# Optimization experiments

Hardware: AMD Instinct MI355X
Metric: run time of the kernel (lower is better)

The kernel has to match this reference:

```python
import jax, jax.numpy as jnp
import numpy as np

B, S, D, H = 4, 2048, 1024, 16
DK = D // H

def setup_inputs() -> dict:
    key = jax.random.key(0)
    ks = jax.random.split(key, 12)
    s = 1.0 / np.sqrt(D)
    return {
        "query": jax.random.normal(ks[0], (B, S, D), jnp.float32),
        "key": jax.random.normal(ks[1], (B, S, D), jnp.float32),
        "value": jax.random.normal(ks[2], (B, S, D), jnp.float32),
        "mask": jax.random.randint(ks[3], (B, S, S), 0, 2, jnp.int32),
        "Wq": jax.random.normal(ks[4], (D, D), jnp.float32) * s,
        "bq": jnp.zeros((D,), jnp.float32),
        "Wk": jax.random.normal(ks[5], (D, D), jnp.float32) * s,
        "bk": jnp.zeros((D,), jnp.float32),
        "Wv": jax.random.normal(ks[6], (D, D), jnp.float32) * s,
        "bv": jnp.zeros((D,), jnp.float32),
        "Wo": jax.random.normal(ks[7], (D, D), jnp.float32) * s,
        "bo": jnp.zeros((D,), jnp.float32),
    }

def _split_heads(x):
    b, s, _ = x.shape
    return x.reshape(b, s, H, DK).transpose(0, 2, 1, 3)  # [b,h,s,dk]

def reference(query, key, value, mask, Wq, bq, Wk, bk, Wv, bv, Wo, bo):
    # torch nn.Linear: y = x @ W.T + b
    Q = _split_heads(query @ Wq.T + bq)
    K = _split_heads(key @ Wk.T + bk)
    V = _split_heads(value @ Wv.T + bv)
    scores = jnp.einsum('bhqd,bhkd->bhqk', Q, K) / np.sqrt(DK)
    scores = jnp.where(mask[:, None, :, :] == 0, jnp.float32(-1e9), scores)
    probs = jax.nn.softmax(scores, axis=-1)
    attn = jnp.einsum('bhqk,bhkd->bhqd', probs, V)
    out = attn.transpose(0, 2, 1, 3).reshape(query.shape[0], -1, H * DK)
    return out @ Wo.T + bo
```

## Files before the change

kernel.cpp:

```cpp
#include <hip/hip_runtime.h>

typedef __attribute__((ext_vector_type(8))) short short8;
typedef __attribute__((ext_vector_type(8))) unsigned short ushort8_t;
typedef __attribute__((ext_vector_type(4))) float floatx4;
typedef __attribute__((ext_vector_type(2))) _Float16 half2_t;
typedef __attribute__((ext_vector_type(4))) _Float16 half4;
typedef __attribute__((ext_vector_type(8))) _Float16 half8;
typedef __attribute__((ext_vector_type(2))) unsigned int uint2v;

#define B_ 4
#define S_ 2048
#define D_ 1024
#define H_ 16
#define DK_ 64
#define BS_ (B_ * S_)
#define XN4_ (BS_ * D_ / 4)
#define WN4_ (D_ * D_ / 4)

union V8u { half8 v8; half4 v4[2]; };
union H16 { _Float16 h; unsigned short u; };

typedef const __attribute__((address_space(1))) void* gvp;
typedef __attribute__((address_space(3))) void* lvp;

static __device__ __forceinline__ unsigned short f2bf(float f) {
  union { float f; unsigned int u; } x; x.f = f;
  unsigned int r = x.u + 0x7fffu + ((x.u >> 16) & 1u);
  return (unsigned short)(r >> 16);
}

static __device__ __forceinline__ half2_t pk_f16(float a, float b) {
  return __builtin_bit_cast(half2_t, __builtin_amdgcn_cvt_pkrtz(a, b));
}

static __device__ __forceinline__ float fexp2(float x) {
  float r;
  asm("v_exp_f32 %0, %1" : "=v"(r) : "v"(x));
  return r;
}

static __device__ __forceinline__ half8 mk8(uint2v a, uint2v b) {
  union { unsigned u[4]; half8 h; } t;
  t.u[0] = a.x; t.u[1] = a.y; t.u[2] = b.x; t.u[3] = b.y;
  return t.h;
}

__global__ void cast_all(const float* __restrict__ q, const float* __restrict__ k,
                         const float* __restrict__ v,
                         const float* __restrict__ wq, const float* __restrict__ wk,
                         const float* __restrict__ wv, const float* __restrict__ wo,
                         unsigned short* __restrict__ oq, unsigned short* __restrict__ ok,
                         unsigned short* __restrict__ ov,
                         unsigned short* __restrict__ owq, unsigned short* __restrict__ owk,
                         unsigned short* __restrict__ owv, unsigned short* __restrict__ owo) {
  int i = blockIdx.x * blockDim.x + threadIdx.x;
  const float* src; unsigned short* dst; int j;
  if (i < 3 * XN4_) {
    int w = i >> 21; j = i & (XN4_ - 1);
    src = (w == 0) ? q : (w == 1) ? k : v;
    dst = (w == 0) ? oq : (w == 1) ? ok : ov;
  } else {
    int t = i - 3 * XN4_;
    int w = t >> 18; j = t & (WN4_ - 1);
    src = (w == 0) ? wq : (w == 1) ? wk : (w == 2) ? wv : wo;
    dst = (w == 0) ? owq : (w == 1) ? owk : (w == 2) ? owv : owo;
  }
  float4 v4 = ((const float4*)src)[j];
  ushort4 o;
  o.x = f2bf(v4.x); o.y = f2bf(v4.y); o.z = f2bf(v4.z); o.w = f2bf(v4.w);
  ((ushort4*)dst)[j] = o;
}

__global__ void pack_mask(const int* __restrict__ mask, unsigned long long* __restrict__ bits) {
  int i = blockIdx.x * blockDim.x + threadIdx.x;
  unsigned long long m = __ballot(mask[i] != 0);
  if ((threadIdx.x & 63) == 0) bits[i >> 6] = m;
}

__device__ __forceinline__ void gemm_core(
    const unsigned short* __restrict__ X, const unsigned short* __restrict__ W,
    const float* __restrict__ bias, void* __restrict__ Y,
    float scale, int mode, int bm, int bn,
    unsigned short* As, unsigned short* Bs)
{
  constexpr int K = D_, N = D_;
  int tid = threadIdx.x;
  int wave = tid >> 6, lane = tid & 63, quad = lane >> 4, li = lane & 15;
  int wm = wave >> 1, wn = wave & 1;
  int srow = lane >> 3;
  int scol = ((lane & 7) ^ srow) * 8;
  const unsigned short* gA = X + (size_t)(bm * 128 + wave * 32 + srow) * K + scol;
  const unsigned short* gB = W + (size_t)(bn * 128 + wave * 32 + srow) * K + scol;

  auto stage = [&](int buf, int k0) {
#pragma unroll
    for (int j = 0; j < 4; ++j) {
      __builtin_amdgcn_global_load_lds((gvp)(gA + (size_t)(j * 8) * K + k0),
          (lvp)(As + buf * 8192 + wave * 2048 + j * 512), 16, 0, 0);
      __builtin_amdgcn_global_load_lds((gvp)(gB + (size_t)(j * 8) * K + k0),
          (lvp)(Bs + buf * 8192 + wave * 2048 + j * 512), 16, 0, 0);
    }
  };

  floatx4 acc[4][4] = {};
  stage(0, 0);
  constexpr int NK = K / 64;
  for (int i = 0; i < NK; ++i) {
    int buf = i & 1;
    __syncthreads();
    if (i + 1 < NK) stage(buf ^ 1, (i + 1) * 64);
    short8 af[2][4], bf[2][4];
#pragma unroll
    for (int s2 = 0; s2 < 2; ++s2)
#pragma unroll
      for (int t = 0; t < 4; ++t) {
        int slot = ((s2 * 4 + quad) ^ (li & 7)) * 8;
        af[s2][t] = *(const short8*)(&As[buf * 8192 + (wm * 64 + t * 16 + li) * 64 + slot]);
        bf[s2][t] = *(const short8*)(&Bs[buf * 8192 + (wn * 64 + t * 16 + li) * 64 + slot]);
      }
#pragma unroll
    for (int s2 = 0; s2 < 2; ++s2)
#pragma unroll
      for (int mt = 0; mt < 4; ++mt)
#pragma unroll
        for (int nt = 0; nt < 4; ++nt)
          acc[mt][nt] = __builtin_amdgcn_mfma_f32_16x16x32_bf16(af[s2][mt], bf[s2][nt], acc[mt][nt], 0, 0, 0);
  }

  if (mode == 3) {
    int mbase = bm * 128 + wm * 64;
    int b0 = mbase >> 11;
    int sblk = mbase & 2047;
#pragma unroll
    for (int nt = 0; nt < 4; ++nt) {
      int n = bn * 128 + wn * 64 + nt * 16 + li;
      float bv = bias[n];
      int h = n >> 6, dk = n & 63;
#pragma unroll
      for (int mt = 0; mt < 4; ++mt) {
        int pos = (mt >> 1) * 32 + quad * 8 + (mt & 1) * 4;
        H16 h0, h1, h2, h3;
        h0.h = (_Float16)(acc[mt][nt][0] + bv);
        h1.h = (_Float16)(acc[mt][nt][1] + bv);
        h2.h = (_Float16)(acc[mt][nt][2] + bv);
        h3.h = (_Float16)(acc[mt][nt][3] + bv);
        uint2v pk;
        pk.x = (unsigned)h0.u | ((unsigned)h1.u << 16);
        pk.y = (unsigned)h2.u | ((unsigned)h3.u << 16);
        size_t idx = (((size_t)(b0 * H_ + h)) * DK_ + dk) * S_ + sblk + pos;
        *(uint2v*)((unsigned short*)Y + idx) = pk;
      }
    }
    return;
  }

#pragma unroll
  for (int nt = 0; nt < 4; ++nt) {
    int n = bn * 128 + wn * 64 + nt * 16 + li;
    float bv = bias[n];
#pragma unroll
    for (int mt = 0; mt < 4; ++mt) {
#pragma unroll
      for (int r = 0; r < 4; ++r) {
        int m = bm * 128 + wm * 64 + mt * 16 + quad * 4 + r;
        float v = (acc[mt][nt][r] + bv) * scale;
        if (mode == 1) {
          ((float*)Y)[(size_t)m * N + n] = v;
        } else {
          int b = m >> 11, s = m & 2047, h = n >> 6, dk = n & 63;
          size_t idx = (((size_t)(b * H_ + h)) * S_ + s) * DK_ + dk;
          ((unsigned short*)Y)[idx] = f2bf(v);
        }
      }
    }
  }
}

__global__ __launch_bounds__(256) void gemm_qkv(
    const unsigned short* __restrict__ Xq, const unsigned short* __restrict__ Xk,
    const unsigned short* __restrict__ Xv,
    const unsigned short* __restrict__ Wq, const unsigned short* __restrict__ Wk,
    const unsigned short* __restrict__ Wv,
    const float* __restrict__ bq, const float* __restrict__ bk, const float* __restrict__ bv,
    unsigned short* __restrict__ Qh, unsigned short* __restrict__ Kh,
    unsigned short* __restrict__ Vt, float sc)
{
  __shared__ __align__(16) unsigned short As[2 * 8192];
  __shared__ __align__(16) unsigned short Bs[2 * 8192];
  int z = blockIdx.z;
  const unsigned short* X = (z == 0) ? Xq : (z == 1) ? Xk : Xv;
  const unsigned short* W = (z == 0) ? Wq : (z == 1) ? Wk : Wv;
  const float* bias = (z == 0) ? bq : (z == 1) ? bk : bv;
  void* Y = (z == 0) ? (void*)Qh : (z == 1) ? (void*)Kh : (void*)Vt;
  float scale = (z == 0) ? sc : 1.0f;
  int mode = (z == 2) ? 3 : 0;
  gemm_core(X, W, bias, Y, scale, mode, blockIdx.y, blockIdx.x, As, Bs);
}

__global__ __launch_bounds__(256) void gemm_out(
    const unsigned short* __restrict__ X, const unsigned short* __restrict__ W,
    const float* __restrict__ bias, float* __restrict__ Y)
{
  __shared__ __align__(16) unsigned short As[2 * 8192];
  __shared__ __align__(16) unsigned short Bs[2 * 8192];
  gemm_core(X, W, bias, Y, 1.0f, 1, blockIdx.y, blockIdx.x, As, Bs);
}

__global__ __launch_bounds__(256) void attn_kernel(
    const unsigned short* __restrict__ Qh,
    const unsigned short* __restrict__ Kh,
    const _Float16* __restrict__ Vt,
    const unsigned long long* __restrict__ mbits,
    unsigned short* __restrict__ attnb)
{
  __shared__ __align__(16) unsigned short Ks[2 * 4096];
  __shared__ __align__(16) unsigned short Vs[2 * 4096];
  __shared__ __align__(8) uint2v mlut[16];

  int tid = threadIdx.x;
  int wave = tid >> 6, lane = tid & 63, quad = lane >> 4, li = lane & 15;

  if (tid < 16) {
    unsigned nb = (unsigned)tid;
    uint2v m;
    m.x = (nb & 1u ? 0x0000FFFFu : 0u) | (nb & 2u ? 0xFFFF0000u : 0u);
    m.y = (nb & 4u ? 0x0000FFFFu : 0u) | (nb & 8u ? 0xFFFF0000u : 0u);
    mlut[nb] = m;
  }

  int blk = blockIdx.x;
  int xcd = blk & 7, slot7 = blk >> 3;
  int bh = xcd * 8 + (slot7 >> 4);
  int qb = slot7 & 15;
  int b = bh >> 4, h = bh & 15;
  int qbase = qb * 128 + wave * 32;
  const size_t hq = (size_t)bh * S_ * DK_;

  short8 aQ[2][2];
#pragma unroll
  for (int qs = 0; qs < 2; ++qs)
#pragma unroll
    for (int s2 = 0; s2 < 2; ++s2)
      aQ[qs][s2] = *(const short8*)(Qh + hq + (size_t)(qbase + qs * 16 + li) * DK_ + s2 * 32 + quad * 8);

  floatx4 o[2][4] = {};
  floatx4 lacc[2] = {};
  const half8 ones8 = {(_Float16)1.f, (_Float16)1.f, (_Float16)1.f, (_Float16)1.f,
                       (_Float16)1.f, (_Float16)1.f, (_Float16)1.f, (_Float16)1.f};

  const unsigned long long* mrow = mbits + ((size_t)b * S_ + qbase + li) * (S_ / 64);

  int srow = lane >> 3;
  int scol = ((lane & 7) ^ srow) * 8;
  const unsigned short* gK = Kh + hq + (size_t)(wave * 16 + srow) * DK_ + scol;
  const _Float16* gV = Vt + ((size_t)bh * 64 + wave * 16 + srow) * S_ + scol;

  auto stage = [&](int buf, int k0) {
#pragma unroll
    for (int j = 0; j < 2; ++j) {
      __builtin_amdgcn_global_load_lds((gvp)(gK + (size_t)(k0 + j * 8) * DK_),
          (lvp)(Ks + buf * 4096 + wave * 1024 + j * 512), 16, 0, 0);
      __builtin_amdgcn_global_load_lds((gvp)(gV + (size_t)(j * 8) * S_ + k0),
          (lvp)(Vs + buf * 4096 + wave * 1024 + j * 512), 16, 0, 0);
    }
  };

  stage(0, 0);
  unsigned long long mw0c = mrow[0];
  unsigned long long mw1c = mrow[16 * (S_ / 64)];

  constexpr int NK = S_ / 64;
#pragma unroll 2
  for (int i = 0; i < NK; ++i) {
    int buf = i & 1;
    __syncthreads();
    if (i + 1 < NK) stage(buf ^ 1, (i + 1) * 64);
    unsigned long long mw0n = 0, mw1n = 0;
    if (i + 1 < NK) { mw0n = mrow[i + 1]; mw1n = mrow[16 * (S_ / 64) + i + 1]; }

    short8 bK[4][2];
#pragma unroll
    for (int t = 0; t < 4; ++t)
#pragma unroll
      for (int s2 = 0; s2 < 2; ++s2)
        bK[t][s2] = *(const short8*)(&Ks[buf * 4096 + (t * 16 + li) * 64 + (((s2 * 4 + quad) ^ (li & 7)) * 8)]);

    V8u vv[4][2];
#pragma unroll
    for (int dt = 0; dt < 4; ++dt)
#pragma unroll
      for (int tp = 0; tp < 2; ++tp)
        vv[dt][tp].v8 = *(const half8*)((const _Float16*)&Vs[buf * 4096 + (dt * 16 + li) * 64 + (((tp * 4 + quad) ^ (li & 7)) * 8)]);

    floatx4 sc[4][2] = {};
    __builtin_amdgcn_s_setprio(1);
#pragma unroll
    for (int s2 = 0; s2 < 2; ++s2)
#pragma unroll
      for (int t = 0; t < 4; ++t)
#pragma unroll
        for (int qs = 0; qs < 2; ++qs)
          sc[t][qs] = __builtin_amdgcn_mfma_f32_16x16x32_bf16(bK[t][s2], aQ[qs][s2], sc[t][qs], 0, 0, 0);
    __builtin_amdgcn_s_setprio(0);

    unsigned long long sh0 = mw0c >> (quad * 4);
    unsigned long long sh1 = mw1c >> (quad * 4);

    uint2v aPu[4][2];
#pragma unroll
    for (int t = 0; t < 4; ++t)
#pragma unroll
      for (int qs = 0; qs < 2; ++qs) {
        unsigned nb = (unsigned)(((qs ? sh1 : sh0) >> (t * 16)) & 15u);
        uint2v mm = mlut[nb];
        float p0 = fexp2(sc[t][qs][0]);
        float p1 = fexp2(sc[t][qs][1]);
        float p2 = fexp2(sc[t][qs][2]);
        float p3 = fexp2(sc[t][qs][3]);
        uint2v pp;
        pp.x = __builtin_bit_cast(unsigned, pk_f16(p0, p1)) & mm.x;
        pp.y = __builtin_bit_cast(unsigned, pk_f16(p2, p3)) & mm.y;
        aPu[t][qs] = pp;
      }

    __builtin_amdgcn_s_setprio(1);
#pragma unroll
    for (int a = 0; a < 2; ++a)
#pragma unroll
      for (int qs = 0; qs < 2; ++qs) {
        half8 pa = mk8(aPu[2 * a][qs], aPu[2 * a + 1][qs]);
        lacc[qs] = __builtin_amdgcn_mfma_f32_16x16x32_f16(pa, ones8, lacc[qs], 0, 0, 0);
#pragma unroll
        for (int dt = 0; dt < 4; ++dt)
          o[qs][dt] = __builtin_amdgcn_mfma_f32_16x16x32_f16(pa, vv[dt][a].v8, o[qs][dt], 0, 0, 0);
      }
    __builtin_amdgcn_s_setprio(0);

    mw0c = mw0n; mw1c = mw1n;
  }

#pragma unroll
  for (int qs = 0; qs < 2; ++qs)
#pragma unroll
    for (int r = 0; r < 4; ++r) {
      float ir = 1.0f / lacc[qs][r];
      size_t row = (size_t)b * S_ + qbase + qs * 16 + quad * 4 + r;
#pragma unroll
      for (int dt = 0; dt < 4; ++dt)
        attnb[row * D_ + h * DK_ + dt * 16 + li] = f2bf(o[qs][dt][r] * ir);
    }
}

extern "C" void kernel_launch(void* const* d_in, const int* in_sizes, int n_in,
                              void* d_out, int out_size, void* d_ws, size_t ws_size,
                              hipStream_t stream) {
  const float* query = (const float*)d_in[0];
  const float* key   = (const float*)d_in[1];
  const float* value = (const float*)d_in[2];
  const int*   mask  = (const int*)d_in[3];
  const float* Wq = (const float*)d_in[4];
  const float* bq = (const float*)d_in[5];
  const float* Wk = (const float*)d_in[6];
  const float* bk = (const float*)d_in[7];
  const float* Wv = (const float*)d_in[8];
  const float* bv = (const float*)d_in[9];
  const float* Wo = (const float*)d_in[10];
  const float* bo = (const float*)d_in[11];
  float* out = (float*)d_out;

  char* ws = (char*)d_ws;
  size_t off = 0;
  auto alloc = [&](size_t bytes) -> void* {
    void* p = ws + off;
    off += (bytes + 255) & ~(size_t)255;
    return p;
  };
  unsigned short* Xq    = (unsigned short*)alloc((size_t)BS_ * D_ * 2);
  unsigned short* Xk    = (unsigned short*)alloc((size_t)BS_ * D_ * 2);
  unsigned short* Xv    = (unsigned short*)alloc((size_t)BS_ * D_ * 2);
  unsigned short* Wqb   = (unsigned short*)alloc((size_t)D_ * D_ * 2);
  unsigned short* Wkb   = (unsigned short*)alloc((size_t)D_ * D_ * 2);
  unsigned short* Wvb   = (unsigned short*)alloc((size_t)D_ * D_ * 2);
  unsigned short* Wob   = (unsigned short*)alloc((size_t)D_ * D_ * 2);
  unsigned short* Qh    = (unsigned short*)alloc((size_t)BS_ * D_ * 2);
  unsigned short* Kh    = (unsigned short*)alloc((size_t)BS_ * D_ * 2);
  unsigned short* Vt    = (unsigned short*)alloc((size_t)BS_ * D_ * 2);
  unsigned short* attnb = (unsigned short*)alloc((size_t)BS_ * D_ * 2);
  unsigned long long* mbits = (unsigned long long*)alloc((size_t)B_ * S_ * (S_ / 64) * 8);

  const float SC = 0.18033688011112042f;

  pack_mask<<<(B_ * S_ * S_) / 256, 256, 0, stream>>>(mask, mbits);

  cast_all<<<(3 * XN4_ + 4 * WN4_) / 256, 256, 0, stream>>>(
      query, key, value, Wq, Wk, Wv, Wo,
      Xq, Xk, Xv, Wqb, Wkb, Wvb, Wob);

  gemm_qkv<<<dim3(D_ / 128, BS_ / 128, 3), 256, 0, stream>>>(
      Xq, Xk, Xv, Wqb, Wkb, Wvb, bq, bk, bv, Qh, Kh, Vt, SC);

  attn_kernel<<<dim3(8 * 8 * 16), 256, 0, stream>>>(Qh, Kh, (const _Float16*)Vt, mbits, attnb);

  gemm_out<<<dim3(D_ / 128, BS_ / 128), 256, 0, stream>>>(attnb, Wob, bo, out);
}
```

Before: 415.2 us.

## Fuse fp32-to-bf16 activation cast into QKV GEMM A-tile staging

Drops the separate cast of the query, key and value activations to bf16. The QKV GEMM now reads fp32 rows straight into registers, converts them with packed bf16 conversion and writes the tile to LDS. The A-tile store is issued after the MFMA loop to overlap with compute. This avoids writing and re-reading three large bf16 intermediates, but the GEMM now reads twice as many A bytes through registers rather than direct global-to-LDS loads, which uses more VGPRs and may hurt latency hiding. The rounding also changes from the manual round-to-nearest-even routine to the hardware packed conversion.

Result: slower. 442.1 us (+6.5%).

```diff
diff --git a/kernel.cpp b/kernel.cpp
--- a/kernel.cpp
+++ b/kernel.cpp
@@ -14,7 +14,6 @@
 #define H_ 16
 #define DK_ 64
 #define BS_ (B_ * S_)
-#define XN4_ (BS_ * D_ / 4)
 #define WN4_ (D_ * D_ / 4)
 
 union V8u { half8 v8; half4 v4[2]; };
@@ -29,6 +28,12 @@
   return (unsigned short)(r >> 16);
 }
 
+static __device__ __forceinline__ unsigned cvtpk_bf16(float a, float b) {
+  unsigned r;
+  asm("v_cvt_pk_bf16_f32 %0, %1, %2" : "=v"(r) : "v"(a), "v"(b));
+  return r;
+}
+
 static __device__ __forceinline__ half2_t pk_f16(float a, float b) {
   return __builtin_bit_cast(half2_t, __builtin_amdgcn_cvt_pkrtz(a, b));
 }
@@ -45,26 +50,14 @@
   return t.h;
 }
 
-__global__ void cast_all(const float* __restrict__ q, const float* __restrict__ k,
-                         const float* __restrict__ v,
-                         const float* __restrict__ wq, const float* __restrict__ wk,
-                         const float* __restrict__ wv, const float* __restrict__ wo,
-                         unsigned short* __restrict__ oq, unsigned short* __restrict__ ok,
-                         unsigned short* __restrict__ ov,
-                         unsigned short* __restrict__ owq, unsigned short* __restrict__ owk,
-                         unsigned short* __restrict__ owv, unsigned short* __restrict__ owo) {
+__global__ void cast_w(const float* __restrict__ wq, const float* __restrict__ wk,
+                       const float* __restrict__ wv, const float* __restrict__ wo,
+                       unsigned short* __restrict__ owq, unsigned short* __restrict__ owk,
+                       unsigned short* __restrict__ owv, unsigned short* __restrict__ owo) {
   int i = blockIdx.x * blockDim.x + threadIdx.x;
-  const float* src; unsigned short* dst; int j;
-  if (i < 3 * XN4_) {
-    int w = i >> 21; j = i & (XN4_ - 1);
-    src = (w == 0) ? q : (w == 1) ? k : v;
-    dst = (w == 0) ? oq : (w == 1) ? ok : ov;
-  } else {
-    int t = i - 3 * XN4_;
-    int w = t >> 18; j = t & (WN4_ - 1);
-    src = (w == 0) ? wq : (w == 1) ? wk : (w == 2) ? wv : wo;
-    dst = (w == 0) ? owq : (w == 1) ? owk : (w == 2) ? owv : owo;
-  }
+  int w = i >> 18, j = i & (WN4_ - 1);
+  const float* src = (w == 0) ? wq : (w == 1) ? wk : (w == 2) ? wv : wo;
+  unsigned short* dst = (w == 0) ? owq : (w == 1) ? owk : (w == 2) ? owv : owo;
   float4 v4 = ((const float4*)src)[j];
   ushort4 o;
   o.x = f2bf(v4.x); o.y = f2bf(v4.y); o.z = f2bf(v4.z); o.w = f2bf(v4.w);
@@ -77,8 +70,9 @@
   if ((threadIdx.x & 63) == 0) bits[i >> 6] = m;
 }
 
+template <bool AF32>
 __device__ __forceinline__ void gemm_core(
-    const unsigned short* __restrict__ X, const unsigned short* __restrict__ W,
+    const void* __restrict__ Xp, const unsigned short* __restrict__ W,
     const float* __restrict__ bias, void* __restrict__ Y,
     float scale, int mode, int bm, int bn,
     unsigned short* As, unsigned short* Bs)
@@ -89,26 +83,57 @@
   int wm = wave >> 1, wn = wave & 1;
   int srow = lane >> 3;
   int scol = ((lane & 7) ^ srow) * 8;
-  const unsigned short* gA = X + (size_t)(bm * 128 + wave * 32 + srow) * K + scol;
+  const unsigned short* gA16 = (const unsigned short*)Xp + (size_t)(bm * 128 + wave * 32 + srow) * K + scol;
+  const float*          gA32 = (const float*)Xp          + (size_t)(bm * 128 + wave * 32 + srow) * K + scol;
   const unsigned short* gB = W + (size_t)(bn * 128 + wave * 32 + srow) * K + scol;
 
-  auto stage = [&](int buf, int k0) {
-#pragma unroll
-    for (int j = 0; j < 4; ++j) {
-      __builtin_amdgcn_global_load_lds((gvp)(gA + (size_t)(j * 8) * K + k0),
-          (lvp)(As + buf * 8192 + wave * 2048 + j * 512), 16, 0, 0);
+  auto stageB = [&](int buf, int k0) {
+#pragma unroll
+    for (int j = 0; j < 4; ++j)
       __builtin_amdgcn_global_load_lds((gvp)(gB + (size_t)(j * 8) * K + k0),
           (lvp)(Bs + buf * 8192 + wave * 2048 + j * 512), 16, 0, 0);
+  };
+  auto stageA16 = [&](int buf, int k0) {
+#pragma unroll
+    for (int j = 0; j < 4; ++j)
+      __builtin_amdgcn_global_load_lds((gvp)(gA16 + (size_t)(j * 8) * K + k0),
+          (lvp)(As + buf * 8192 + wave * 2048 + j * 512), 16, 0, 0);
+  };
+
+  float4 fa0[4], fa1[4];
+  auto loadA32 = [&](int k0) {
+#pragma unroll
+    for (int j = 0; j < 4; ++j) {
+      fa0[j] = *(const float4*)(gA32 + (size_t)(j * 8) * K + k0);
+      fa1[j] = *(const float4*)(gA32 + (size_t)(j * 8) * K + k0 + 4);
+    }
+  };
+  auto writeA32 = [&](int buf) {
+#pragma unroll
+    for (int j = 0; j < 4; ++j) {
+      uint4 p;
+      p.x = cvtpk_bf16(fa0[j].x, fa0[j].y);
+      p.y = cvtpk_bf16(fa0[j].z, fa0[j].w);
+      p.z = cvtpk_bf16(fa1[j].x, fa1[j].y);
+      p.w = cvtpk_bf16(fa1[j].z, fa1[j].w);
+      *(uint4*)(&As[buf * 8192 + wave * 2048 + j * 512 + lane * 8]) = p;
     }
   };
 
   floatx4 acc[4][4] = {};
-  stage(0, 0);
+  stageB(0, 0);
+  if (AF32) { loadA32(0); writeA32(0); }
+  else stageA16(0, 0);
+
   constexpr int NK = K / 64;
   for (int i = 0; i < NK; ++i) {
     int buf = i & 1;
     __syncthreads();
-    if (i + 1 < NK) stage(buf ^ 1, (i + 1) * 64);
+    if (i + 1 < NK) {
+      stageB(buf ^ 1, (i + 1) * 64);
+      if (AF32) loadA32((i + 1) * 64);
+      else stageA16(buf ^ 1, (i + 1) * 64);
+    }
     short8 af[2][4], bf[2][4];
 #pragma unroll
     for (int s2 = 0; s2 < 2; ++s2)
@@ -125,6 +150,7 @@
 #pragma unroll
         for (int nt = 0; nt < 4; ++nt)
           acc[mt][nt] = __builtin_amdgcn_mfma_f32_16x16x32_bf16(af[s2][mt], bf[s2][nt], acc[mt][nt], 0, 0, 0);
+    if (AF32 && i + 1 < NK) writeA32(buf ^ 1);
   }
 
   if (mode == 3) {
@@ -177,8 +203,8 @@
 }
 
 __global__ __launch_bounds__(256) void gemm_qkv(
-    const unsigned short* __restrict__ Xq, const unsigned short* __restrict__ Xk,
-    const unsigned short* __restrict__ Xv,
+    const float* __restrict__ Xq, const float* __restrict__ Xk,
+    const float* __restrict__ Xv,
     const unsigned short* __restrict__ Wq, const unsigned short* __restrict__ Wk,
     const unsigned short* __restrict__ Wv,
     const float* __restrict__ bq, const float* __restrict__ bk, const float* __restrict__ bv,
@@ -188,13 +214,13 @@
   __shared__ __align__(16) unsigned short As[2 * 8192];
   __shared__ __align__(16) unsigned short Bs[2 * 8192];
   int z = blockIdx.z;
-  const unsigned short* X = (z == 0) ? Xq : (z == 1) ? Xk : Xv;
+  const float* X = (z == 0) ? Xq : (z == 1) ? Xk : Xv;
   const unsigned short* W = (z == 0) ? Wq : (z == 1) ? Wk : Wv;
   const float* bias = (z == 0) ? bq : (z == 1) ? bk : bv;
   void* Y = (z == 0) ? (void*)Qh : (z == 1) ? (void*)Kh : (void*)Vt;
   float scale = (z == 0) ? sc : 1.0f;
   int mode = (z == 2) ? 3 : 0;
-  gemm_core(X, W, bias, Y, scale, mode, blockIdx.y, blockIdx.x, As, Bs);
+  gemm_core<true>((const void*)X, W, bias, Y, scale, mode, blockIdx.y, blockIdx.x, As, Bs);
 }
 
 __global__ __launch_bounds__(256) void gemm_out(
@@ -203,7 +229,7 @@
 {
   __shared__ __align__(16) unsigned short As[2 * 8192];
   __shared__ __align__(16) unsigned short Bs[2 * 8192];
-  gemm_core(X, W, bias, Y, 1.0f, 1, blockIdx.y, blockIdx.x, As, Bs);
+  gemm_core<false>((const void*)X, W, bias, Y, 1.0f, 1, blockIdx.y, blockIdx.x, As, Bs);
 }
 
 __global__ __launch_bounds__(256) void attn_kernel(
@@ -375,9 +401,6 @@
     off += (bytes + 255) & ~(size_t)255;
     return p;
   };
-  unsigned short* Xq    = (unsigned short*)alloc((size_t)BS_ * D_ * 2);
-  unsigned short* Xk    = (unsigned short*)alloc((size_t)BS_ * D_ * 2);
-  unsigned short* Xv    = (unsigned short*)alloc((size_t)BS_ * D_ * 2);
   unsigned short* Wqb   = (unsigned short*)alloc((size_t)D_ * D_ * 2);
   unsigned short* Wkb   = (unsigned short*)alloc((size_t)D_ * D_ * 2);
   unsigned short* Wvb   = (unsigned short*)alloc((size_t)D_ * D_ * 2);
@@ -392,12 +415,10 @@
 
   pack_mask<<<(B_ * S_ * S_) / 256, 256, 0, stream>>>(mask, mbits);
 
-  cast_all<<<(3 * XN4_ + 4 * WN4_) / 256, 256, 0, stream>>>(
-      query, key, value, Wq, Wk, Wv, Wo,
-      Xq, Xk, Xv, Wqb, Wkb, Wvb, Wob);
+  cast_w<<<(4 * WN4_) / 256, 256, 0, stream>>>(Wq, Wk, Wv, Wo, Wqb, Wkb, Wvb, Wob);
 
   gemm_qkv<<<dim3(D_ / 128, BS_ / 128, 3), 256, 0, stream>>>(
-      Xq, Xk, Xv, Wqb, Wkb, Wvb, bq, bk, bv, Qh, Kh, Vt, SC);
+      query, key, value, Wqb, Wkb, Wvb, bq, bk, bv, Qh, Kh, Vt, SC);
 
   attn_kernel<<<dim3(8 * 8 * 16), 256, 0, stream>>>(Qh, Kh, (const _Float16*)Vt, mbits, attnb);
 
```
